# Optimization experiments

Hardware: AMD Instinct MI355X
Metric: run time of the kernel (lower is better)

The kernel has to match this reference:

```python
import jax, jax.numpy as jnp
import numpy as np

PS = 8          # patch size
E = 8           # experts per layer
L = 2           # PCE layers
F = 4           # fourier frequencies -> pos channels = 2+4F = 18
TEMP = 1.0
GROUPS = 4
B, H, W, CS, NCLS = 64, 128, 128, 8, 100
P = (H // PS) * (W // PS)
N = B * P
CAP = int(np.ceil(1.25 * N / E))  # expert capacity
POSC = 2 + 4 * F


def conv3x3(x, w):
    return jax.lax.conv_general_dilated(x, w, (1, 1), 'SAME',
                                        dimension_numbers=('NCHW', 'OIHW', 'NCHW'))


def patchify(x, ps):
    b, c, h, w = x.shape
    hp, wp = h // ps, w // ps
    t = x.reshape(b, c, hp, ps, wp, ps).transpose(0, 2, 4, 1, 3, 5)
    return t.reshape(b * hp * wp, c, ps, ps), hp, wp


def unpatchify(t, b, hp, wp):
    n, c, ph, pw = t.shape
    return t.reshape(b, hp, wp, c, ph, pw).transpose(0, 3, 1, 4, 2, 5).reshape(b, c, hp * ph, wp * pw)


def fourier_pos(h, w, f):
    yy, xx = jnp.meshgrid(jnp.linspace(-1., 1., h), jnp.linspace(-1., 1., w), indexing='ij')
    feats = [yy, xx]
    for k in range(f):
        fr = jnp.pi * (2.0 ** k)
        feats += [jnp.sin(fr * yy), jnp.cos(fr * yy), jnp.sin(fr * xx), jnp.cos(fr * xx)]
    return jnp.stack(feats, 0)  # [2+4F, H, W]


def group_norm(x, s, b, groups=GROUPS, eps=1e-5):
    n, c, h, w = x.shape
    xg = x.reshape(n, groups, c // groups, h, w)
    mu = xg.mean((2, 3, 4), keepdims=True)
    var = xg.var((2, 3, 4), keepdims=True)
    xg = (xg - mu) / jnp.sqrt(var + eps)
    return xg.reshape(n, c, h, w) * s[None, :, None, None] + b[None, :, None, None]


def setup_inputs():
    key = jax.random.key(0)
    ks = jax.random.split(key, 8)
    return {
        'X': jax.random.normal(ks[0], (B, 3, H, W), jnp.float32),
        'stem_w': jax.random.normal(ks[1], (CS, 3, 3, 3), jnp.float32) * 0.1,
        'stem_scale': jnp.ones((CS,), jnp.float32),
        'stem_bias': jnp.zeros((CS,), jnp.float32),
        'gate_w': jax.random.normal(ks[2], (L, POSC, E), jnp.float32) * 0.1,
        'gate_b': jnp.zeros((L, E), jnp.float32),
        'exp_w': jax.random.normal(ks[3], (L, E, CS, CS, 3, 3), jnp.float32) * 0.05,
        'exp_b': jnp.zeros((L, E, CS), jnp.float32),
        'gn_scale': jnp.ones((L, CS), jnp.float32),
        'gn_bias': jnp.zeros((L, CS), jnp.float32),
        'head_w1': jax.random.normal(ks[4], (CS, 4 * CS), jnp.float32) * 0.1,
        'head_b1': jnp.zeros((4 * CS,), jnp.float32),
        'head_w2': jax.random.normal(ks[5], (4 * CS, NCLS), jnp.float32) * 0.1,
        'head_b2': jnp.zeros((NCLS,), jnp.float32),
    }


def reference(X, stem_w, stem_scale, stem_bias, gate_w, gate_b, exp_w, exp_b,
              gn_scale, gn_bias, head_w1, head_b1, head_w2, head_b2):
    b = X.shape[0]
    # stem: conv + (folded) BN affine + SiLU
    x = jax.nn.silu(conv3x3(X, stem_w) * stem_scale[None, :, None, None]
                    + stem_bias[None, :, None, None])
    tokens, hp, wp = patchify(x, PS)                       # [N, CS, PS, PS]
    pos = fourier_pos(x.shape[2], x.shape[3], F)           # [POSC, H, W]
    pos_p, _, _ = patchify(pos[None], PS)                  # [P, POSC, PS, PS]
    pos_pool = jnp.tile(pos_p.mean((2, 3)), (b, 1))        # [N, POSC]

    tot_z = jnp.float32(0.)
    tot_imb = jnp.float32(0.)
    for l in range(L):
        logits = pos_pool @ gate_w[l] + gate_b[l]          # [N, E]
        probs = jax.nn.softmax(logits / TEMP, axis=-1)
        tot_z = tot_z + jnp.mean(jax.nn.logsumexp(logits, axis=-1) ** 2)
        e_idx = jnp.argmax(probs, axis=-1)                 # top-1 expert per token
        oh = jax.nn.one_hot(e_idx, E, dtype=jnp.float32)
        slot = (jnp.sum(jnp.cumsum(oh, axis=0) * oh, axis=1) - 1.).astype(jnp.int32)
        keep = slot < CAP
        frac = jnp.mean(oh * keep[:, None].astype(jnp.float32), axis=0)
        tot_imb = tot_imb + E * jnp.sum(jnp.mean(probs, axis=0) * frac)
        gate = jnp.take_along_axis(probs, e_idx[:, None], axis=1)[:, 0] * keep.astype(probs.dtype)
        e_safe = jnp.where(keep, e_idx, E)                 # OOB index -> dropped
        einp = jnp.zeros((E, CAP) + tokens.shape[1:], tokens.dtype)
        einp = einp.at[e_safe, slot].set(tokens, mode='drop')   # dispatch gather
        eout = jax.vmap(lambda xi, wi, bi: jax.nn.silu(conv3x3(xi, wi)
                        + bi[None, :, None, None]))(einp, exp_w[l], exp_b[l])
        out = eout[e_idx, jnp.minimum(slot, CAP - 1)] * gate[:, None, None, None]
        if l == L - 1:
            x = group_norm(unpatchify(out, b, hp, wp), gn_scale[l], gn_bias[l])
        else:
            tokens = group_norm(out, gn_scale[l], gn_bias[l])

    pooled = x.mean((2, 3))                                # AdaptiveAvgPool2d(1)+flatten
    h1 = jax.nn.gelu(pooled @ head_w1 + head_b1)
    logits_out = h1 @ head_w2 + head_b2
    return logits_out, tot_z, tot_imb
```

## Files before the change

kernel.cpp:

```cpp
#include <hip/hip_runtime.h>
#include <math.h>

#define CAPV 2560

typedef __bf16 bf16x8 __attribute__((ext_vector_type(8)));
typedef float f32x4 __attribute__((ext_vector_type(4)));

__device__ __forceinline__ float wave_sum64(float v) {
#pragma unroll
  for (int o = 32; o; o >>= 1) v += __shfl_xor(v, o, 64);
  return v;
}

__device__ __forceinline__ float silu_f(float t) {
  return t * __builtin_amdgcn_rcpf(1.f + __expf(-t));
}

__device__ __forceinline__ unsigned short f2bf(float f) {
  unsigned u = __float_as_uint(f);
  return (unsigned short)((u + 0x7FFFu + ((u >> 16) & 1u)) >> 16);
}

__global__ __launch_bounds__(256) void routing_kernel(
    const float* __restrict__ gate_w, const float* __restrict__ gate_b,
    const float* __restrict__ stem_w, const float* __restrict__ exp_w,
    int* __restrict__ route_e, float* __restrict__ route_gate,
    int* __restrict__ route_cpre, int* __restrict__ route_Ce,
    float* __restrict__ stemT2, unsigned short* __restrict__ expPack,
    float* __restrict__ d_scalars) {
  const int tid = threadIdx.x;
  if (blockIdx.x > 0) {
    int le = blockIdx.x - 1;
    for (int i = tid; i < 1536; i += 256) {
      int c = i >> 9, rem = i & 511, ln = rem >> 3, j = rem & 7;
      int k = c * 32 + ((ln >> 4) << 3) + j;
      int cl = ln & 15;
      int tap = k >> 3, ci = k & 7;
      int dy = tap >> 2, dx = tap & 3;
      float v = 0.f;
      if (cl < 8 && dx < 3)
        v = exp_w[((le * 8 + cl) * 8 + ci) * 9 + dy * 3 + dx];
      expPack[le * 1536 + i] = f2bf(v);
    }
    return;
  }
  if (tid < 216) {
    int co = tid / 27, r2 = tid % 27;
    int ci = r2 / 9, t = r2 % 9;
    stemT2[(ci * 8 + co) * 12 + t] = stem_w[tid];
  }

  __shared__ float tS[128][4], tC[128][4];
  __shared__ float sS8[16][4], sC8[16][4];
  if (tid < 128) {
    float yv = -1.f + (2.f / 127.f) * (float)tid;
#pragma unroll
    for (int k = 0; k < 4; ++k) {
      float fr = 3.14159265358979323846f * (float)(1 << k);
      tS[tid][k] = sinf(fr * yv);
      tC[tid][k] = cosf(fr * yv);
    }
  }
  __syncthreads();
  if (tid < 64) {
    int g8 = tid >> 2, k = tid & 3;
    float s = 0.f, c = 0.f;
#pragma unroll
    for (int r = 0; r < 8; ++r) {
      s += tS[g8 * 8 + r][k];
      c += tC[g8 * 8 + r][k];
    }
    sS8[g8][k] = s * 0.125f;
    sC8[g8][k] = c * 0.125f;
  }
  __syncthreads();

  const int p = tid;
  const int lane = p & 63, wv = p >> 6;
  const int hp = p >> 4, wp = p & 15;

  float pool[18];
  pool[0] = -1.f + (2.f / 127.f) * ((float)(hp * 8) + 3.5f);
  pool[1] = -1.f + (2.f / 127.f) * ((float)(wp * 8) + 3.5f);
#pragma unroll
  for (int k = 0; k < 4; ++k) {
    pool[2 + 4 * k] = sS8[hp][k];
    pool[3 + 4 * k] = sC8[hp][k];
    pool[4 + 4 * k] = sS8[wp][k];
    pool[5 + 4 * k] = sC8[wp][k];
  }

  __shared__ float sWP[4][8];
  __shared__ float sWZ[4];
  __shared__ int sWCnt[4][8];
  __shared__ float sMeanP[8], sFrac[8];
  __shared__ float sAcc[2];
  if (p == 0) { sAcc[0] = 0.f; sAcc[1] = 0.f; }

  for (int l = 0; l < 2; ++l) {
    float logit[8];
#pragma unroll
    for (int e = 0; e < 8; ++e) logit[e] = gate_b[l * 8 + e];
#pragma unroll
    for (int c = 0; c < 18; ++c) {
      float pl = pool[c];
#pragma unroll
      for (int e = 0; e < 8; ++e)
        logit[e] = fmaf(pl, gate_w[(l * 18 + c) * 8 + e], logit[e]);
    }
    float mxv = logit[0]; int em = 0;
#pragma unroll
    for (int e = 1; e < 8; ++e)
      if (logit[e] > mxv) { mxv = logit[e]; em = e; }
    float pr[8]; float se = 0.f;
#pragma unroll
    for (int e = 0; e < 8; ++e) { pr[e] = expf(logit[e] - mxv); se += pr[e]; }
    float inv = 1.f / se;
#pragma unroll
    for (int e = 0; e < 8; ++e) pr[e] *= inv;
    float lse = mxv + logf(se);
    float gate_val = inv;

    unsigned long long meq[8];
#pragma unroll
    for (int e = 0; e < 8; ++e) meq[e] = __ballot(em == e);
    unsigned long long mm = meq[0];
#pragma unroll
    for (int e = 1; e < 8; ++e) mm = (em == e) ? meq[e] : mm;
    unsigned long long below = (2ull << lane) - 1ull;
    int cpre_w = (int)__popcll(mm & below);
    if (lane < 8) {
      unsigned long long t = meq[0];
#pragma unroll
      for (int e = 1; e < 8; ++e) t = (lane == e) ? meq[e] : t;
      sWCnt[wv][lane] = (int)__popcll(t);
    }
    float z2 = wave_sum64(lse * lse);
    if (lane == 0) sWZ[wv] = z2;
#pragma unroll
    for (int e = 0; e < 8; ++e) {
      float s = wave_sum64(pr[e]);
      if (lane == 0) sWP[wv][e] = s;
    }
    __syncthreads();

    int cpre = cpre_w;
#pragma unroll
    for (int w2 = 0; w2 < 4; ++w2)
      if (w2 < wv) cpre += sWCnt[w2][em];

    route_e[l * 256 + p] = em;
    route_gate[l * 256 + p] = gate_val;
    route_cpre[l * 256 + p] = cpre;

    if (p < 8) {
      int ce = sWCnt[0][p] + sWCnt[1][p] + sWCnt[2][p] + sWCnt[3][p];
      route_Ce[l * 8 + p] = ce;
      int kept = 0;
      for (int bb = 0; bb < 64; ++bb) {
        int r = CAPV - bb * ce;
        r = r < 0 ? 0 : r;
        kept += (r < ce ? r : ce);
      }
      sFrac[p] = (float)kept * (1.f / 16384.f);
      sMeanP[p] = (sWP[0][p] + sWP[1][p] + sWP[2][p] + sWP[3][p]) * (1.f / 256.f);
    }
    __syncthreads();
    if (p == 0) {
      float s = 0.f;
#pragma unroll
      for (int e = 0; e < 8; ++e) s += sMeanP[e] * sFrac[e];
      sAcc[1] += 8.f * s;
      sAcc[0] += (sWZ[0] + sWZ[1] + sWZ[2] + sWZ[3]) * (1.f / 256.f);
    }
    __syncthreads();
  }
  if (p == 0) { d_scalars[0] = sAcc[0]; d_scalars[1] = sAcc[1]; }
}

__global__ __launch_bounds__(256) void token_kernel(
    const float* __restrict__ X,
    const float* __restrict__ stemT2, const float* __restrict__ stem_sc,
    const float* __restrict__ stem_bi,
    const unsigned short* __restrict__ expPack, const float* __restrict__ exp_b,
    const float* __restrict__ gn_s, const float* __restrict__ gn_b,
    const int* __restrict__ route_e, const float* __restrict__ route_gate,
    const int* __restrict__ route_cpre, const int* __restrict__ route_Ce,
    float* __restrict__ blk_sums) {
  const int g = blockIdx.x;
  const int b = g >> 6, r6 = g & 63;
  const int hp = r6 >> 2, wq = r6 & 3;
  const int tid = threadIdx.x;
  const int w = tid >> 6, lane = tid & 63;
  const int p = hp * 16 + wq * 4 + w;

  __shared__ __align__(16) float sX[3][10][36];
  __shared__ __align__(16) unsigned short sT[4][10][12][8];
  __shared__ float sRed[4][12];

  const int e0 = __builtin_amdgcn_readfirstlane(route_e[p]);
  const int e1 = __builtin_amdgcn_readfirstlane(route_e[256 + p]);
  const float gp0 = route_gate[p], gp1 = route_gate[256 + p];
  const int cp0 = route_cpre[p], cp1 = route_cpre[256 + p];
  const int Ce0 = route_Ce[e0], Ce1 = route_Ce[8 + e1];
  const float gate0 = (b * Ce0 + cp0 <= CAPV) ? gp0 : 0.f;
  const float gate1 = (b * Ce1 + cp1 <= CAPV) ? gp1 : 0.f;
  const int le0 = e0, le1 = 8 + e1;
  const bf16x8* bp0 = (const bf16x8*)(expPack + le0 * 1536);
  const bf16x8* bp1 = (const bf16x8*)(expPack + le1 * 1536);
  bf16x8 B00 = bp0[lane], B01 = bp0[64 + lane], B02 = bp0[128 + lane];
  bf16x8 B10 = bp1[lane], B11 = bp1[64 + lane], B12 = bp1[128 + lane];

  if (lane < 56) {
    int row, col;
    if (lane < 12) { row = 0; col = lane; }
    else if (lane < 24) { row = 9; col = lane - 12; }
    else { int q = lane - 24; row = 1 + (q >> 2); int m = q & 3; col = (m == 0) ? 0 : 8 + m; }
    int4 z = {0, 0, 0, 0};
    *(int4*)&sT[w][row][col][0] = z;
  }

  const int gy0 = hp * 8 - 1, gx0 = wq * 32 - 1;
#pragma unroll
  for (int k = 0; k < 4; ++k) {
    int i = tid + k * 256;
    if (i < 1020) {
      int ci = i / 340, rem = i - ci * 340;
      int r = rem / 34, c = rem - r * 34;
      int gy = gy0 + r, gx = gx0 + c;
      float v = 0.f;
      if (gy >= 0 && gy < 128 && gx >= 0 && gx < 128)
        v = X[((b * 3 + ci) * 128 + gy) * 128 + gx];
      sX[ci][r][c] = v;
    }
  }
  __syncthreads();

  {
    const int sy = lane >> 3, sco = lane & 7;
    const int xb = w * 8;
    float acc[8];
#pragma unroll
    for (int px = 0; px < 8; ++px) acc[px] = 0.f;
#pragma unroll
    for (int ci = 0; ci < 3; ++ci) {
      float r[3][10];
#pragma unroll
      for (int dy = 0; dy < 3; ++dy) {
        const float* rp = &sX[ci][sy + dy][xb];
        float4 q0 = *(const float4*)rp;
        float4 q1 = *(const float4*)(rp + 4);
        float2 q2 = *(const float2*)(rp + 8);
        r[dy][0] = q0.x; r[dy][1] = q0.y; r[dy][2] = q0.z; r[dy][3] = q0.w;
        r[dy][4] = q1.x; r[dy][5] = q1.y; r[dy][6] = q1.z; r[dy][7] = q1.w;
        r[dy][8] = q2.x; r[dy][9] = q2.y;
      }
      const float* wp = stemT2 + (ci * 8 + sco) * 12;
      float4 wa = *(const float4*)wp;
      float4 wbv = *(const float4*)(wp + 4);
      float w8 = wp[8];
      float ws9[9] = {wa.x, wa.y, wa.z, wa.w, wbv.x, wbv.y, wbv.z, wbv.w, w8};
#pragma unroll
      for (int dy = 0; dy < 3; ++dy)
#pragma unroll
        for (int dx = 0; dx < 3; ++dx) {
          float wv = ws9[dy * 3 + dx];
#pragma unroll
          for (int px = 0; px < 8; ++px)
            acc[px] = fmaf(wv, r[dy][px + dx], acc[px]);
        }
    }
    float sc = stem_sc[sco], bi = stem_bi[sco];
#pragma unroll
    for (int px = 0; px < 8; ++px) {
      float t = silu_f(fmaf(acc[px], sc, bi));
      sT[w][sy + 1][px + 1][sco] = f2bf(t);
    }
  }

  const int col = lane & 15;
  const int gq = lane >> 4;
  const int ay = (lane & 15) >> 3;
  const int ax = lane & 7;
  const unsigned short* abase = &sT[w][ay][ax + gq][0];
  const float sgs0 = gn_s[col & 7], sgb0 = gn_b[col & 7];
  const float bias0 = exp_b[le0 * 8 + (col & 7)];
  const float bias1 = exp_b[le1 * 8 + (col & 7)];

  const int dy_ = (gq >> 1) + 1, dx_ = (gq & 1) * 4 + 1;

  float v1s, v1q;
  {
    f32x4 a0 = {0.f, 0.f, 0.f, 0.f}, a1 = a0, a2 = a0, a3 = a0;
#pragma unroll
    for (int c = 0; c < 3; ++c) {
      const bf16x8 A0 = *(const bf16x8*)(abase + (c * 2 + 0) * 96);
      const bf16x8 A1 = *(const bf16x8*)(abase + (c * 2 + 2) * 96 - c * 96);
      const bf16x8 Ar0 = *(const bf16x8*)(abase + (0 * 192 + c * 96));
      const bf16x8 Ar1 = *(const bf16x8*)(abase + (1 * 192 + c * 96));
      const bf16x8 Ar2 = *(const bf16x8*)(abase + (2 * 192 + c * 96));
      const bf16x8 Ar3 = *(const bf16x8*)(abase + (3 * 192 + c * 96));
      const bf16x8 Bc = (c == 0) ? B00 : (c == 1) ? B01 : B02;
      a0 = __builtin_amdgcn_mfma_f32_16x16x32_bf16(Ar0, Bc, a0, 0, 0, 0);
      a1 = __builtin_amdgcn_mfma_f32_16x16x32_bf16(Ar1, Bc, a1, 0, 0, 0);
      a2 = __builtin_amdgcn_mfma_f32_16x16x32_bf16(Ar2, Bc, a2, 0, 0, 0);
      a3 = __builtin_amdgcn_mfma_f32_16x16x32_bf16(Ar3, Bc, a3, 0, 0, 0);
      (void)A0; (void)A1;
    }
    float v[16];
    float s = 0.f, q = 0.f;
#pragma unroll
    for (int rg = 0; rg < 4; ++rg) {
      f32x4 ar = (rg == 0) ? a0 : (rg == 1) ? a1 : (rg == 2) ? a2 : a3;
#pragma unroll
      for (int r = 0; r < 4; ++r) {
        float t = silu_f(ar[r] + bias0) * gate0;
        v[rg * 4 + r] = t;
        s += t;
        q += t * t;
      }
    }
    s += __shfl_xor(s, 16, 64); q += __shfl_xor(q, 16, 64);
    s += __shfl_xor(s, 32, 64); q += __shfl_xor(q, 32, 64);
    s += __shfl_xor(s, 1, 64);  q += __shfl_xor(q, 1, 64);
    float mu = s * (1.f / 128.f);
    float var = q * (1.f / 128.f) - mu * mu;
    float inv = rsqrtf(var + 1e-5f);
    float sc2 = inv * sgs0;
    float bi2 = fmaf(-mu, sc2, sgb0);
    if (col < 8) {
#pragma unroll
      for (int rg = 0; rg < 4; ++rg)
#pragma unroll
        for (int r = 0; r < 4; ++r) {
          float n = fmaf(v[rg * 4 + r], sc2, bi2);
          sT[w][rg * 2 + dy_][dx_ + r][col] = f2bf(n);
        }
    }
  }
  {
    f32x4 a0 = {0.f, 0.f, 0.f, 0.f}, a1 = a0, a2 = a0, a3 = a0;
#pragma unroll
    for (int c = 0; c < 3; ++c) {
      const bf16x8 Ar0 = *(const bf16x8*)(abase + (0 * 192 + c * 96));
      const bf16x8 Ar1 = *(const bf16x8*)(abase + (1 * 192 + c * 96));
      const bf16x8 Ar2 = *(const bf16x8*)(abase + (2 * 192 + c * 96));
      const bf16x8 Ar3 = *(const bf16x8*)(abase + (3 * 192 + c * 96));
      const bf16x8 Bc = (c == 0) ? B10 : (c == 1) ? B11 : B12;
      a0 = __builtin_amdgcn_mfma_f32_16x16x32_bf16(Ar0, Bc, a0, 0, 0, 0);
      a1 = __builtin_amdgcn_mfma_f32_16x16x32_bf16(Ar1, Bc, a1, 0, 0, 0);
      a2 = __builtin_amdgcn_mfma_f32_16x16x32_bf16(Ar2, Bc, a2, 0, 0, 0);
      a3 = __builtin_amdgcn_mfma_f32_16x16x32_bf16(Ar3, Bc, a3, 0, 0, 0);
    }
    float s = 0.f, q = 0.f;
#pragma unroll
    for (int rg = 0; rg < 4; ++rg) {
      f32x4 ar = (rg == 0) ? a0 : (rg == 1) ? a1 : (rg == 2) ? a2 : a3;
#pragma unroll
      for (int r = 0; r < 4; ++r) {
        float t = silu_f(ar[r] + bias1) * gate1;
        s += t;
        q += t * t;
      }
    }
    s += __shfl_xor(s, 16, 64); q += __shfl_xor(q, 16, 64);
    s += __shfl_xor(s, 32, 64); q += __shfl_xor(q, 32, 64);
    v1s = s;
    v1q = q + __shfl_xor(q, 1, 64);
  }

  if (lane < 8) sRed[w][lane] = v1s;
  if (lane < 8 && !(lane & 1)) sRed[w][8 + (lane >> 1)] = v1q;
  __syncthreads();
  if (tid < 12)
    blk_sums[(size_t)g * 12 + tid] =
        sRed[0][tid] + sRed[1][tid] + sRed[2][tid] + sRed[3][tid];
}

__global__ __launch_bounds__(64) void finish_kernel(
    const float* __restrict__ blk_sums,
    const float* __restrict__ gn_s, const float* __restrict__ gn_b,
    const float* __restrict__ w1, const float* __restrict__ b1,
    const float* __restrict__ w2, const float* __restrict__ b2,
    float* __restrict__ out) {
  const int b = blockIdx.x;
  const int lane = threadIdx.x;

  const float4* s4 = (const float4*)(blk_sums + (size_t)(b * 64 + lane) * 12);
  float4 a0 = s4[0], a1 = s4[1], a2 = s4[2];
  float l0[12] = {a0.x, a0.y, a0.z, a0.w, a1.x, a1.y, a1.z, a1.w,
                  a2.x, a2.y, a2.z, a2.w};
#pragma unroll
  for (int j = 0; j < 12; ++j) l0[j] = wave_sum64(l0[j]);

  float pooled[8];
#pragma unroll
  for (int c = 0; c < 8; ++c) {
    int gg = c >> 1;
    float mean_c = l0[c] * (1.f / 16384.f);
    float mug = (l0[2 * gg] + l0[2 * gg + 1]) * (1.f / 32768.f);
    float var = l0[8 + gg] * (1.f / 32768.f) - mug * mug;
    pooled[c] = fmaf((mean_c - mug) * rsqrtf(var + 1e-5f), gn_s[8 + c], gn_b[8 + c]);
  }

  __shared__ float sH1[32];
  if (lane < 32) {
    float h = b1[lane];
#pragma unroll
    for (int c = 0; c < 8; ++c) h = fmaf(pooled[c], w1[c * 32 + lane], h);
    float t = 0.7978845608028654f * fmaf(0.044715f * h * h, h, h);
    sH1[lane] = 0.5f * h * (1.f + tanhf(t));
  }
  __syncthreads();
  for (int o = lane; o < 100; o += 64) {
    float v = b2[o];
#pragma unroll
    for (int j = 0; j < 32; ++j) v = fmaf(sH1[j], w2[j * 100 + o], v);
    out[b * 100 + o] = v;
  }
}

extern "C" void kernel_launch(void* const* d_in, const int* in_sizes, int n_in,
                              void* d_out, int out_size, void* d_ws, size_t ws_size,
                              hipStream_t stream) {
  const float* X       = (const float*)d_in[0];
  const float* stem_w  = (const float*)d_in[1];
  const float* stem_sc = (const float*)d_in[2];
  const float* stem_bi = (const float*)d_in[3];
  const float* gate_w  = (const float*)d_in[4];
  const float* gate_b  = (const float*)d_in[5];
  const float* exp_w   = (const float*)d_in[6];
  const float* exp_b   = (const float*)d_in[7];
  const float* gn_s    = (const float*)d_in[8];
  const float* gn_b    = (const float*)d_in[9];
  const float* w1      = (const float*)d_in[10];
  const float* b1      = (const float*)d_in[11];
  const float* w2      = (const float*)d_in[12];
  const float* b2      = (const float*)d_in[13];
  float* out = (float*)d_out;

  char* ws = (char*)d_ws;
  int* route_e             = (int*)(ws + 0);
  int* route_cpre          = (int*)(ws + 2048);
  int* route_Ce            = (int*)(ws + 4096);
  float* route_gate        = (float*)(ws + 4160);
  float* stemT2            = (float*)(ws + 8192);
  unsigned short* expPack  = (unsigned short*)(ws + 16384);
  float* blk_sums          = (float*)(ws + 65536);

  routing_kernel<<<17, 256, 0, stream>>>(gate_w, gate_b, stem_w, exp_w,
                                         route_e, route_gate, route_cpre,
                                         route_Ce, stemT2, expPack, out + 6400);
  token_kernel<<<4096, 256, 0, stream>>>(X, stemT2, stem_sc, stem_bi, expPack,
                                         exp_b, gn_s, gn_b, route_e, route_gate,
                                         route_cpre, route_Ce, blk_sums);
  finish_kernel<<<64, 64, 0, stream>>>(blk_sums, gn_s, gn_b, w1, b1, w2, b2,
                                       out);
}
```

Baseline: 51.89 us.

## Compute stem 3x3 conv with bf16 MFMA instead of scalar FP32 FMAs

The stem convolution now runs as bf16 MFMA (16x16x32) using a packed weight matrix that is prepared in the routing kernel, with stem_scale folded into the weights. The input tile is staged in shared memory as bf16 in a channel-last layout padded to 8 channels, which needs an extra zero-fill and barrier. This removes the per-lane scalar FMA loop over 27 taps. The cost is lower stem precision (bf16 inputs and weights) and extra shared-memory setup. Manual rounding helpers are replaced by native __bf16 casts.

```diff
diff --git a/kernel.cpp b/kernel.cpp
--- a/kernel.cpp
+++ b/kernel.cpp
@@ -16,17 +16,13 @@
   return t * __builtin_amdgcn_rcpf(1.f + __expf(-t));
 }
 
-__device__ __forceinline__ unsigned short f2bf(float f) {
-  unsigned u = __float_as_uint(f);
-  return (unsigned short)((u + 0x7FFFu + ((u >> 16) & 1u)) >> 16);
-}
-
 __global__ __launch_bounds__(256) void routing_kernel(
     const float* __restrict__ gate_w, const float* __restrict__ gate_b,
-    const float* __restrict__ stem_w, const float* __restrict__ exp_w,
+    const float* __restrict__ stem_w, const float* __restrict__ stem_sc,
+    const float* __restrict__ exp_w,
     int* __restrict__ route_e, float* __restrict__ route_gate,
     int* __restrict__ route_cpre, int* __restrict__ route_Ce,
-    float* __restrict__ stemT2, unsigned short* __restrict__ expPack,
+    __bf16* __restrict__ stemPack, __bf16* __restrict__ expPack,
     float* __restrict__ d_scalars) {
   const int tid = threadIdx.x;
   if (blockIdx.x > 0) {
@@ -40,14 +36,20 @@
       float v = 0.f;
       if (cl < 8 && dx < 3)
         v = exp_w[((le * 8 + cl) * 8 + ci) * 9 + dy * 3 + dx];
-      expPack[le * 1536 + i] = f2bf(v);
+      expPack[le * 1536 + i] = (__bf16)v;
     }
     return;
   }
-  if (tid < 216) {
-    int co = tid / 27, r2 = tid % 27;
-    int ci = r2 / 9, t = r2 % 9;
-    stemT2[(ci * 8 + co) * 12 + t] = stem_w[tid];
+  for (int i = tid; i < 1536; i += 256) {
+    int c = i >> 9, rem = i & 511, ln = rem >> 3, j = rem & 7;
+    int k = c * 32 + ((ln >> 4) << 3) + j;
+    int cl = ln & 15;
+    int tap = k >> 3, ci = k & 7;
+    int dy = tap >> 2, dx = tap & 3;
+    float v = 0.f;
+    if (cl < 8 && dx < 3 && ci < 3)
+      v = stem_w[(cl * 3 + ci) * 9 + dy * 3 + dx] * stem_sc[cl];
+    stemPack[i] = (__bf16)v;
   }
 
   __shared__ float tS[128][4], tC[128][4];
@@ -180,9 +182,8 @@
 
 __global__ __launch_bounds__(256) void token_kernel(
     const float* __restrict__ X,
-    const float* __restrict__ stemT2, const float* __restrict__ stem_sc,
-    const float* __restrict__ stem_bi,
-    const unsigned short* __restrict__ expPack, const float* __restrict__ exp_b,
+    const __bf16* __restrict__ stemPack, const float* __restrict__ stem_bi,
+    const __bf16* __restrict__ expPack, const float* __restrict__ exp_b,
     const float* __restrict__ gn_s, const float* __restrict__ gn_b,
     const int* __restrict__ route_e, const float* __restrict__ route_gate,
     const int* __restrict__ route_cpre, const int* __restrict__ route_Ce,
@@ -194,8 +195,14 @@
   const int w = tid >> 6, lane = tid & 63;
   const int p = hp * 16 + wq * 4 + w;
 
-  __shared__ __align__(16) float sX[3][10][36];
-  __shared__ __align__(16) unsigned short sT[4][10][12][8];
+  const int col = lane & 15;
+  const int gq = lane >> 4;
+  const int ay = (lane & 15) >> 3;
+  const int ax = lane & 7;
+  const int dy_ = (gq >> 1) + 1, dx_ = (gq & 1) * 4 + 1;
+
+  __shared__ __align__(16) __bf16 sH[10][36][8];
+  __shared__ __align__(16) __bf16 sT[4][10][12][8];
   __shared__ float sRed[4][12];
 
   const int e0 = __builtin_amdgcn_readfirstlane(route_e[p]);
@@ -203,22 +210,34 @@
   const float gp0 = route_gate[p], gp1 = route_gate[256 + p];
   const int cp0 = route_cpre[p], cp1 = route_cpre[256 + p];
   const int Ce0 = route_Ce[e0], Ce1 = route_Ce[8 + e1];
-  const float gate0 = (b * Ce0 + cp0 <= CAPV) ? gp0 : 0.f;
-  const float gate1 = (b * Ce1 + cp1 <= CAPV) ? gp1 : 0.f;
+  const float gate0 = (col < 8 && b * Ce0 + cp0 <= CAPV) ? gp0 : 0.f;
+  const float gate1 = (col < 8 && b * Ce1 + cp1 <= CAPV) ? gp1 : 0.f;
   const int le0 = e0, le1 = 8 + e1;
+  const bf16x8* sp = (const bf16x8*)stemPack;
   const bf16x8* bp0 = (const bf16x8*)(expPack + le0 * 1536);
   const bf16x8* bp1 = (const bf16x8*)(expPack + le1 * 1536);
+  bf16x8 SB0 = sp[lane], SB1 = sp[64 + lane], SB2 = sp[128 + lane];
   bf16x8 B00 = bp0[lane], B01 = bp0[64 + lane], B02 = bp0[128 + lane];
   bf16x8 B10 = bp1[lane], B11 = bp1[64 + lane], B12 = bp1[128 + lane];
 
+  {
+    float4 z4 = {0.f, 0.f, 0.f, 0.f};
+    float4* h4 = (float4*)&sH[0][0][0];
+#pragma unroll
+    for (int i = 0; i < 2; ++i) {
+      int idx = tid + i * 256;
+      if (idx < 360) h4[idx] = z4;
+    }
+  }
   if (lane < 56) {
-    int row, col;
-    if (lane < 12) { row = 0; col = lane; }
-    else if (lane < 24) { row = 9; col = lane - 12; }
-    else { int q = lane - 24; row = 1 + (q >> 2); int m = q & 3; col = (m == 0) ? 0 : 8 + m; }
+    int row, c2;
+    if (lane < 12) { row = 0; c2 = lane; }
+    else if (lane < 24) { row = 9; c2 = lane - 12; }
+    else { int q = lane - 24; row = 1 + (q >> 2); int m = q & 3; c2 = (m == 0) ? 0 : 8 + m; }
     int4 z = {0, 0, 0, 0};
-    *(int4*)&sT[w][row][col][0] = z;
-  }
+    *(int4*)&sT[w][row][c2][0] = z;
+  }
+  __syncthreads();
 
   const int gy0 = hp * 8 - 1, gx0 = wq * 32 - 1;
 #pragma unroll
@@ -228,84 +247,60 @@
       int ci = i / 340, rem = i - ci * 340;
       int r = rem / 34, c = rem - r * 34;
       int gy = gy0 + r, gx = gx0 + c;
-      float v = 0.f;
       if (gy >= 0 && gy < 128 && gx >= 0 && gx < 128)
-        v = X[((b * 3 + ci) * 128 + gy) * 128 + gx];
-      sX[ci][r][c] = v;
+        sH[r][c][ci] = (__bf16)X[((b * 3 + ci) * 128 + gy) * 128 + gx];
     }
   }
   __syncthreads();
 
   {
-    const int sy = lane >> 3, sco = lane & 7;
-    const int xb = w * 8;
-    float acc[8];
-#pragma unroll
-    for (int px = 0; px < 8; ++px) acc[px] = 0.f;
-#pragma unroll
-    for (int ci = 0; ci < 3; ++ci) {
-      float r[3][10];
-#pragma unroll
-      for (int dy = 0; dy < 3; ++dy) {
-        const float* rp = &sX[ci][sy + dy][xb];
-        float4 q0 = *(const float4*)rp;
-        float4 q1 = *(const float4*)(rp + 4);
-        float2 q2 = *(const float2*)(rp + 8);
-        r[dy][0] = q0.x; r[dy][1] = q0.y; r[dy][2] = q0.z; r[dy][3] = q0.w;
-        r[dy][4] = q1.x; r[dy][5] = q1.y; r[dy][6] = q1.z; r[dy][7] = q1.w;
-        r[dy][8] = q2.x; r[dy][9] = q2.y;
+    const float bias = stem_bi[col & 7];
+    f32x4 d0 = {0.f, 0.f, 0.f, 0.f}, d1 = d0, d2 = d0, d3 = d0;
+#pragma unroll
+    for (int c = 0; c < 3; ++c) {
+      const __bf16* ab = &sH[ay + c][w * 8 + ax + gq][0];
+      bf16x8 A0 = *(const bf16x8*)(ab);
+      bf16x8 A1 = *(const bf16x8*)(ab + 576);
+      bf16x8 A2 = *(const bf16x8*)(ab + 1152);
+      bf16x8 A3 = *(const bf16x8*)(ab + 1728);
+      bf16x8 Bc = (c == 0) ? SB0 : (c == 1) ? SB1 : SB2;
+      d0 = __builtin_amdgcn_mfma_f32_16x16x32_bf16(A0, Bc, d0, 0, 0, 0);
+      d1 = __builtin_amdgcn_mfma_f32_16x16x32_bf16(A1, Bc, d1, 0, 0, 0);
+      d2 = __builtin_amdgcn_mfma_f32_16x16x32_bf16(A2, Bc, d2, 0, 0, 0);
+      d3 = __builtin_amdgcn_mfma_f32_16x16x32_bf16(A3, Bc, d3, 0, 0, 0);
+    }
+    if (col < 8) {
+#pragma unroll
+      for (int rg = 0; rg < 4; ++rg) {
+        f32x4 dr = (rg == 0) ? d0 : (rg == 1) ? d1 : (rg == 2) ? d2 : d3;
+#pragma unroll
+        for (int r = 0; r < 4; ++r) {
+          float t = silu_f(dr[r] + bias);
+          sT[w][rg * 2 + dy_][dx_ + r][col] = (__bf16)t;
+        }
       }
-      const float* wp = stemT2 + (ci * 8 + sco) * 12;
-      float4 wa = *(const float4*)wp;
-      float4 wbv = *(const float4*)(wp + 4);
-      float w8 = wp[8];
-      float ws9[9] = {wa.x, wa.y, wa.z, wa.w, wbv.x, wbv.y, wbv.z, wbv.w, w8};
-#pragma unroll
-      for (int dy = 0; dy < 3; ++dy)
-#pragma unroll
-        for (int dx = 0; dx < 3; ++dx) {
-          float wv = ws9[dy * 3 + dx];
-#pragma unroll
-          for (int px = 0; px < 8; ++px)
-            acc[px] = fmaf(wv, r[dy][px + dx], acc[px]);
-        }
-    }
-    float sc = stem_sc[sco], bi = stem_bi[sco];
-#pragma unroll
-    for (int px = 0; px < 8; ++px) {
-      float t = silu_f(fmaf(acc[px], sc, bi));
-      sT[w][sy + 1][px + 1][sco] = f2bf(t);
-    }
-  }
-
-  const int col = lane & 15;
-  const int gq = lane >> 4;
-  const int ay = (lane & 15) >> 3;
-  const int ax = lane & 7;
-  const unsigned short* abase = &sT[w][ay][ax + gq][0];
-  const float sgs0 = gn_s[col & 7], sgb0 = gn_b[col & 7];
+    }
+  }
+
+  const __bf16* abase = &sT[w][ay][ax + gq][0];
   const float bias0 = exp_b[le0 * 8 + (col & 7)];
   const float bias1 = exp_b[le1 * 8 + (col & 7)];
-
-  const int dy_ = (gq >> 1) + 1, dx_ = (gq & 1) * 4 + 1;
+  const float sgs0 = gn_s[col & 7], sgb0 = gn_b[col & 7];
 
   float v1s, v1q;
   {
     f32x4 a0 = {0.f, 0.f, 0.f, 0.f}, a1 = a0, a2 = a0, a3 = a0;
 #pragma unroll
     for (int c = 0; c < 3; ++c) {
-      const bf16x8 A0 = *(const bf16x8*)(abase + (c * 2 + 0) * 96);
-      const bf16x8 A1 = *(const bf16x8*)(abase + (c * 2 + 2) * 96 - c * 96);
-      const bf16x8 Ar0 = *(const bf16x8*)(abase + (0 * 192 + c * 96));
-      const bf16x8 Ar1 = *(const bf16x8*)(abase + (1 * 192 + c * 96));
-      const bf16x8 Ar2 = *(const bf16x8*)(abase + (2 * 192 + c * 96));
-      const bf16x8 Ar3 = *(const bf16x8*)(abase + (3 * 192 + c * 96));
-      const bf16x8 Bc = (c == 0) ? B00 : (c == 1) ? B01 : B02;
-      a0 = __builtin_amdgcn_mfma_f32_16x16x32_bf16(Ar0, Bc, a0, 0, 0, 0);
-      a1 = __builtin_amdgcn_mfma_f32_16x16x32_bf16(Ar1, Bc, a1, 0, 0, 0);
-      a2 = __builtin_amdgcn_mfma_f32_16x16x32_bf16(Ar2, Bc, a2, 0, 0, 0);
-      a3 = __builtin_amdgcn_mfma_f32_16x16x32_bf16(Ar3, Bc, a3, 0, 0, 0);
-      (void)A0; (void)A1;
+      bf16x8 A0 = *(const bf16x8*)(abase + (0 * 192 + c * 96));
+      bf16x8 A1 = *(const bf16x8*)(abase + (1 * 192 + c * 96));
+      bf16x8 A2 = *(const bf16x8*)(abase + (2 * 192 + c * 96));
+      bf16x8 A3 = *(const bf16x8*)(abase + (3 * 192 + c * 96));
+      bf16x8 Bc = (c == 0) ? B00 : (c == 1) ? B01 : B02;
+      a0 = __builtin_amdgcn_mfma_f32_16x16x32_bf16(A0, Bc, a0, 0, 0, 0);
+      a1 = __builtin_amdgcn_mfma_f32_16x16x32_bf16(A1, Bc, a1, 0, 0, 0);
+      a2 = __builtin_amdgcn_mfma_f32_16x16x32_bf16(A2, Bc, a2, 0, 0, 0);
+      a3 = __builtin_amdgcn_mfma_f32_16x16x32_bf16(A3, Bc, a3, 0, 0, 0);
     }
     float v[16];
     float s = 0.f, q = 0.f;
@@ -334,7 +329,7 @@
 #pragma unroll
         for (int r = 0; r < 4; ++r) {
           float n = fmaf(v[rg * 4 + r], sc2, bi2);
-          sT[w][rg * 2 + dy_][dx_ + r][col] = f2bf(n);
+          sT[w][rg * 2 + dy_][dx_ + r][col] = (__bf16)n;
         }
     }
   }
@@ -342,15 +337,15 @@
     f32x4 a0 = {0.f, 0.f, 0.f, 0.f}, a1 = a0, a2 = a0, a3 = a0;
 #pragma unroll
     for (int c = 0; c < 3; ++c) {
-      const bf16x8 Ar0 = *(const bf16x8*)(abase + (0 * 192 + c * 96));
-      const bf16x8 Ar1 = *(const bf16x8*)(abase + (1 * 192 + c * 96));
-      const bf16x8 Ar2 = *(const bf16x8*)(abase + (2 * 192 + c * 96));
-      const bf16x8 Ar3 = *(const bf16x8*)(abase + (3 * 192 + c * 96));
-      const bf16x8 Bc = (c == 0) ? B10 : (c == 1) ? B11 : B12;
-      a0 = __builtin_amdgcn_mfma_f32_16x16x32_bf16(Ar0, Bc, a0, 0, 0, 0);
-      a1 = __builtin_amdgcn_mfma_f32_16x16x32_bf16(Ar1, Bc, a1, 0, 0, 0);
-      a2 = __builtin_amdgcn_mfma_f32_16x16x32_bf16(Ar2, Bc, a2, 0, 0, 0);
-      a3 = __builtin_amdgcn_mfma_f32_16x16x32_bf16(Ar3, Bc, a3, 0, 0, 0);
+      bf16x8 A0 = *(const bf16x8*)(abase + (0 * 192 + c * 96));
+      bf16x8 A1 = *(const bf16x8*)(abase + (1 * 192 + c * 96));
+      bf16x8 A2 = *(const bf16x8*)(abase + (2 * 192 + c * 96));
+      bf16x8 A3 = *(const bf16x8*)(abase + (3 * 192 + c * 96));
+      bf16x8 Bc = (c == 0) ? B10 : (c == 1) ? B11 : B12;
+      a0 = __builtin_amdgcn_mfma_f32_16x16x32_bf16(A0, Bc, a0, 0, 0, 0);
+      a1 = __builtin_amdgcn_mfma_f32_16x16x32_bf16(A1, Bc, a1, 0, 0, 0);
+      a2 = __builtin_amdgcn_mfma_f32_16x16x32_bf16(A2, Bc, a2, 0, 0, 0);
+      a3 = __builtin_amdgcn_mfma_f32_16x16x32_bf16(A3, Bc, a3, 0, 0, 0);
     }
     float s = 0.f, q = 0.f;
 #pragma unroll
@@ -440,19 +435,19 @@
   float* out = (float*)d_out;
 
   char* ws = (char*)d_ws;
-  int* route_e             = (int*)(ws + 0);
-  int* route_cpre          = (int*)(ws + 2048);
-  int* route_Ce            = (int*)(ws + 4096);
-  float* route_gate        = (float*)(ws + 4160);
-  float* stemT2            = (float*)(ws + 8192);
-  unsigned short* expPack  = (unsigned short*)(ws + 16384);
-  float* blk_sums          = (float*)(ws + 65536);
-
-  routing_kernel<<<17, 256, 0, stream>>>(gate_w, gate_b, stem_w, exp_w,
+  int* route_e      = (int*)(ws + 0);
+  int* route_cpre   = (int*)(ws + 2048);
+  int* route_Ce     = (int*)(ws + 4096);
+  float* route_gate = (float*)(ws + 4160);
+  __bf16* stemPack  = (__bf16*)(ws + 8192);
+  __bf16* expPack   = (__bf16*)(ws + 16384);
+  float* blk_sums   = (float*)(ws + 65536);
+
+  routing_kernel<<<17, 256, 0, stream>>>(gate_w, gate_b, stem_w, stem_sc, exp_w,
                                          route_e, route_gate, route_cpre,
-                                         route_Ce, stemT2, expPack, out + 6400);
-  token_kernel<<<4096, 256, 0, stream>>>(X, stemT2, stem_sc, stem_bi, expPack,
-                                         exp_b, gn_s, gn_b, route_e, route_gate,
+                                         route_Ce, stemPack, expPack, out + 6400);
+  token_kernel<<<4096, 256, 0, stream>>>(X, stemPack, stem_bi, expPack, exp_b,
+                                         gn_s, gn_b, route_e, route_gate,
                                          route_cpre, route_Ce, blk_sums);
   finish_kernel<<<64, 64, 0, stream>>>(blk_sums, gn_s, gn_b, w1, b1, w2, b2,
                                        out);
```

New measurement: 51.39 us (median of 2 runs). Within noise of the previous version (-1.0%).
